# Kernel optimization log

Measured on AMD Instinct MI355X. Metric: run time of the kernel, lower is better.

Reference implementation:

```python
import jax, jax.numpy as jnp
import numpy as np

D_MODEL = 1024
N_HEADS = 16
HEAD = D_MODEL // N_HEADS  # 64


def setup_inputs() -> dict:
    key = jax.random.key(0)
    ks = jax.random.split(key, 9)
    s = 1.0 / np.sqrt(D_MODEL)
    x = jax.random.normal(ks[0], (2, 2048, D_MODEL), dtype=jnp.float32)
    Wq = jax.random.uniform(ks[1], (N_HEADS, D_MODEL, HEAD), jnp.float32, -s, s)
    bq = jax.random.uniform(ks[2], (N_HEADS, HEAD), jnp.float32, -s, s)
    Wk = jax.random.uniform(ks[3], (N_HEADS, D_MODEL, HEAD), jnp.float32, -s, s)
    bk = jax.random.uniform(ks[4], (N_HEADS, HEAD), jnp.float32, -s, s)
    Wv = jax.random.uniform(ks[5], (N_HEADS, D_MODEL, HEAD), jnp.float32, -s, s)
    bv = jax.random.uniform(ks[6], (N_HEADS, HEAD), jnp.float32, -s, s)
    Wo = jax.random.uniform(ks[7], (D_MODEL, D_MODEL), jnp.float32, -s, s)
    bo = jax.random.uniform(ks[8], (D_MODEL,), jnp.float32, -s, s)
    return {"x": x, "Wq": Wq, "bq": bq, "Wk": Wk, "bk": bk,
            "Wv": Wv, "bv": bv, "Wo": Wo, "bo": bo}


def reference(x, Wq, bq, Wk, bk, Wv, bv, Wo, bo):
    # Per-head projections, vectorized over heads: [B,S,D] x [H,D,h] -> [B,H,S,h]
    Q = jnp.einsum('bsd,hdk->bhsk', x, Wq) + bq[None, :, None, :]
    K = jnp.einsum('bsd,hdk->bhsk', x, Wk) + bk[None, :, None, :]
    V = jnp.einsum('bsd,hdk->bhsk', x, Wv) + bv[None, :, None, :]
    scores = jnp.einsum('bhqk,bhsk->bhqs', Q, K) / jnp.sqrt(jnp.float32(HEAD))
    attn = jax.nn.softmax(scores, axis=-1)  # dropout is identity in eval mode
    out = jnp.einsum('bhqs,bhsk->bhqk', attn, V)  # [B,H,S,h]
    B, H, S, h = out.shape
    out = out.transpose(0, 2, 1, 3).reshape(B, S, H * h)  # concat heads -> [B,S,D]
    return out @ Wo.T + bo if False else jnp.einsum('bsd,ed->bse', out, Wo.T.T) + bo
```

## Files before the change

kernel.cpp:

```cpp
#include <hip/hip_runtime.h>
#include <hip/hip_bf16.h>

typedef unsigned short u16;
typedef short short8 __attribute__((ext_vector_type(8)));
typedef float floatx4 __attribute__((ext_vector_type(4)));

#define MFMA16(a, b, c) __builtin_amdgcn_mfma_f32_16x16x32_bf16((a), (b), (c), 0, 0, 0)

union U128u { uint4 q; u16 s[8]; };

__device__ __forceinline__ u16 f2bf(float f) {
  union { float f; unsigned u; } v; v.f = f;
  unsigned r = v.u + 0x7fffu + ((v.u >> 16) & 1u);
  return (u16)(r >> 16);
}

__device__ __forceinline__ float bf2f(u16 s) {
  union { unsigned u; float f; } v; v.u = ((unsigned)s) << 16;
  return v.f;
}

__device__ __forceinline__ unsigned pk2(float hi, float lo) {
  union { float f; unsigned u; } a, b;
  a.f = hi; b.f = lo;
  return __builtin_amdgcn_perm(a.u + 0x8000u, b.u + 0x8000u, 0x07060302u);
}

__device__ __forceinline__ float fexp2(float x) {
#if __has_builtin(__builtin_amdgcn_exp2f)
  return __builtin_amdgcn_exp2f(x);
#else
  return exp2f(x);
#endif
}

__device__ __forceinline__ void async16(const u16* g, u16* l) {
  __builtin_amdgcn_global_load_lds(
      (const __attribute__((address_space(1))) unsigned int*)g,
      (__attribute__((address_space(3))) unsigned int*)l, 16, 0, 0);
}


__global__ __launch_bounds__(256) void prep_all(
    const float* __restrict__ x, const float* __restrict__ Wo,
    const float* __restrict__ Wq, const float* __restrict__ bq,
    const float* __restrict__ Wk, const float* __restrict__ bk,
    const float* __restrict__ Wv, const float* __restrict__ bv,
    u16* __restrict__ Xb, u16* __restrict__ Wob,
    u16* __restrict__ Wt, float* __restrict__ ball) {
  int bid = blockIdx.x;
  int tid = threadIdx.x;
  if (bid < 5120) {
    const float* src = bid < 4096 ? x : Wo;
    u16* dst = bid < 4096 ? Xb : Wob;
    int i = (bid < 4096 ? bid : bid - 4096) * 256 + tid;
    float4 v = ((const float4*)src)[i];
    union { unsigned long long ll; u16 s[4]; } o;
    o.s[0] = f2bf(v.x); o.s[1] = f2bf(v.y); o.s[2] = f2bf(v.z); o.s[3] = f2bf(v.w);
    ((unsigned long long*)dst)[i] = o.ll;
    return;
  }
  int id = (bid - 5120) * 256 + tid;
  int kk4 = id & 15;
  int d = (id >> 4) & 1023;
  int h = (id >> 14) & 15;
  int wsel = id >> 18;
  const float* W = wsel == 0 ? Wq : (wsel == 1 ? Wk : Wv);
  float4 v = *(const float4*)(W + ((size_t)(h * 1024 + d)) * 64 + kk4 * 4);
  int nb = wsel * 1024 + h * 64 + kk4 * 4;
  Wt[(size_t)(nb + 0) * 1024 + d] = f2bf(v.x);
  Wt[(size_t)(nb + 1) * 1024 + d] = f2bf(v.y);
  Wt[(size_t)(nb + 2) * 1024 + d] = f2bf(v.z);
  Wt[(size_t)(nb + 3) * 1024 + d] = f2bf(v.w);
  if (id < 3072) {
    int ws2 = id >> 10, hk = id & 1023;
    const float* bsrc = ws2 == 0 ? bq : (ws2 == 1 ? bk : bv);
    ball[id] = bsrc[hk];
  }
}


__device__ __forceinline__ void store_out(u16* p, float v) { *p = f2bf(v); }
__device__ __forceinline__ void store_out(float* p, float v) { *p = v; }

template <int BN, bool SPLITV, bool TRANS, typename OutT>
__global__ __launch_bounds__(256, 4) void gemm_bt(
    const u16* __restrict__ A, const u16* __restrict__ B,
    const float* __restrict__ bias, OutT* __restrict__ C,
    u16* __restrict__ Vtc,
    int M, int N, int K, int scaleNend, float scaleVal) {
  constexpr int TN = BN / 32;
  __shared__ __attribute__((aligned(16))) u16 As[128 * 64];
  __shared__ __attribute__((aligned(16))) u16 Bs[BN * 64];
  const int tid = threadIdx.x;
  const int w = tid >> 6, lane = tid & 63;
  const int l15 = lane & 15, l4 = lane >> 4;
  const int lin = blockIdx.x;
  const int xcd = lin & 7, sblk = lin >> 3;
  const int bm = xcd * 4 + (sblk & 3);
  const int bn = sblk >> 2;
  const int wm = (w & 1) * 64, wn = (w >> 1) * (BN / 2);

  floatx4 acc[4][TN];
#pragma unroll
  for (int i = 0; i < 4; ++i)
#pragma unroll
    for (int j = 0; j < TN; ++j) acc[i][j] = (floatx4){0.f, 0.f, 0.f, 0.f};

  for (int k0 = 0; k0 < K; k0 += 64) {
    __syncthreads();
#pragma unroll
    for (int j = 0; j < 4; ++j) {
      int i = j * 256 + tid;
      int row = i >> 3, c = (i & 7) ^ (row & 7);
      async16(A + (size_t)(bm * 128 + row) * K + k0 + c * 8, As + (j * 256 + w * 64) * 8);
    }
#pragma unroll
    for (int j = 0; j < BN / 32; ++j) {
      int i = j * 256 + tid;
      int row = i >> 3, c = (i & 7) ^ (row & 7);
      async16(B + (size_t)(bn * BN + row) * K + k0 + c * 8, Bs + (j * 256 + w * 64) * 8);
    }
    __syncthreads();
    const int sw = l15 & 7;
#pragma unroll
    for (int ks = 0; ks < 2; ++ks) {
      short8 af[4], bf[TN];
#pragma unroll
      for (int t = 0; t < 4; ++t)
        af[t] = *(const short8*)(As + (wm + t * 16 + l15) * 64 + (((ks * 4 + l4) ^ sw)) * 8);
#pragma unroll
      for (int t = 0; t < TN; ++t)
        bf[t] = *(const short8*)(Bs + (wn + t * 16 + l15) * 64 + (((ks * 4 + l4) ^ sw)) * 8);
#pragma unroll
      for (int tm = 0; tm < 4; ++tm)
#pragma unroll
        for (int tn = 0; tn < TN; ++tn)
          acc[tm][tn] = TRANS ? MFMA16(bf[tn], af[tm], acc[tm][tn])
                              : MFMA16(af[tm], bf[tn], acc[tm][tn]);
    }
  }

  if (TRANS) {
#pragma unroll
    for (int tn = 0; tn < TN; ++tn) {
      int colb = bn * BN + wn + tn * 16 + l4 * 4;
      float4 bv4 = *(const float4*)(bias + colb);
#pragma unroll
      for (int tm = 0; tm < 4; ++tm) {
        int row = bm * 128 + wm + tm * 16 + l15;
        float4 v;
        v.x = acc[tm][tn][0] + bv4.x;
        v.y = acc[tm][tn][1] + bv4.y;
        v.z = acc[tm][tn][2] + bv4.z;
        v.w = acc[tm][tn][3] + bv4.w;
        *(float4*)((float*)C + (size_t)row * N + colb) = v;
      }
    }
    return;
  }

#pragma unroll
  for (int tn = 0; tn < TN; ++tn) {
    int col = bn * BN + wn + tn * 16 + l15;
    float bv = bias[col];
    float sc = (col < scaleNend) ? scaleVal : 1.0f;
    if (!SPLITV || col < 2048) {
#pragma unroll
      for (int tm = 0; tm < 4; ++tm) {
        int row0 = bm * 128 + wm + tm * 16 + l4 * 4;
#pragma unroll
        for (int r = 0; r < 4; ++r) {
          float v = (acc[tm][tn][r] + bv) * sc;
          store_out(C + (size_t)(row0 + r) * N + col, v);
        }
      }
    } else {
      int hv = (col - 2048) >> 6, d = (col - 2048) & 63;
#pragma unroll
      for (int tm = 0; tm < 4; ++tm) {
        int row0 = bm * 128 + wm + tm * 16 + l4 * 4;
        int bb = row0 >> 11, s0 = row0 & 2047;
        union { unsigned long long ll; u16 s[4]; } o;
#pragma unroll
        for (int r = 0; r < 4; ++r) o.s[r] = f2bf(acc[tm][tn][r] + bv);
        size_t idx = ((((size_t)(bb * 16 + hv) * 128 + (s0 >> 4)) * 2 + ((s0 >> 3) & 1)) * 64 + d) * 8 +
                     (s0 & 7);
        *(unsigned long long*)(Vtc + idx) = o.ll;
      }
    }
  }
}

__global__ __launch_bounds__(256, 3) void attn_kernel(const u16* __restrict__ QKV,
                                                      const u16* __restrict__ Vtc,
                                                      u16* __restrict__ Ob) {
  __shared__ __attribute__((aligned(16))) u16 lds[4 * 5120];
  const int tid = threadIdx.x;
  const int w = tid >> 6, lane = tid & 63;
  const int l15 = lane & 15, l4 = lane >> 4;
  const int lin = blockIdx.x;
  const int xcd = lin & 7, sblk = lin >> 3;
  const int bh = xcd * 4 + (sblk & 3);
  const int q0 = (sblk >> 2) * 64;
  const int b = bh >> 4, h = bh & 15;

  u16* const Pw = lds + w * 5120;

  short8 qf[4][2];
  {
    const u16* Qb = QKV + (size_t)(b * 2048 + q0) * 3072 + h * 64;
#pragma unroll
    for (int tq = 0; tq < 4; ++tq)
#pragma unroll
      for (int s = 0; s < 2; ++s)
        qf[tq][s] = *(const short8*)(Qb + (size_t)(tq * 16 + l15) * 3072 + s * 32 + l4 * 8);
  }

  floatx4 Oacc[4][4];
#pragma unroll
  for (int i = 0; i < 4; ++i)
#pragma unroll
    for (int j = 0; j < 4; ++j) Oacc[i][j] = (floatx4){0.f, 0.f, 0.f, 0.f};
  float lpart[4] = {0.f, 0.f, 0.f, 0.f};

  const u16* const Kb = QKV + (size_t)(b * 2048) * 3072 + 1024 + h * 64;
  const u16* const Vw = Vtc + (size_t)bh * 131072 + (size_t)w * 32768;
  const int kw0 = w * 512;

  auto do_st = [&](int c, u16* pb) {
    const int key0 = kw0 + c * 32;
    short8 kf[2][2];
#pragma unroll
    for (int t = 0; t < 2; ++t)
#pragma unroll
      for (int s = 0; s < 2; ++s)
        kf[t][s] = *(const short8*)(Kb + (size_t)(key0 + t * 16 + l15) * 3072 + s * 32 + l4 * 8);
#pragma unroll
    for (int t = 0; t < 2; ++t)
#pragma unroll
      for (int tq = 0; tq < 4; ++tq) {
        floatx4 s = (floatx4){0.f, 0.f, 0.f, 0.f};
        s = MFMA16(kf[t][0], qf[tq][0], s);
        s = MFMA16(kf[t][1], qf[tq][1], s);
        float p0 = fexp2(s[0]), p1 = fexp2(s[1]), p2 = fexp2(s[2]), p3 = fexp2(s[3]);
        lpart[tq] += (p0 + p1) + (p2 + p3);
        unsigned lo = pk2(p1, p0), hi = pk2(p3, p2);
        *(unsigned long long*)(pb + (size_t)(tq * 16 + l15) * 40 + t * 16 + l4 * 4) =
            ((unsigned long long)hi << 32) | lo;
      }
  };

  auto do_pv = [&](int c, const u16* pb) {
    short8 vf[4];
#pragma unroll
    for (int td = 0; td < 4; ++td)
      vf[td] = *(const short8*)(Vw + (size_t)c * 2048 + l4 * 512 + (td * 16 + l15) * 8);
    short8 pf[4];
#pragma unroll
    for (int tq = 0; tq < 4; ++tq)
      pf[tq] = *(const short8*)(pb + (size_t)(tq * 16 + l15) * 40 + l4 * 8);
#pragma unroll
    for (int td = 0; td < 4; ++td)
#pragma unroll
      for (int tq = 0; tq < 4; ++tq) Oacc[tq][td] = MFMA16(pf[tq], vf[td], Oacc[tq][td]);
  };

  do_st(0, Pw);
#pragma unroll 1
  for (int c = 1; c < 16; ++c) {
    do_st(c, Pw + (c & 1) * 2560);
    do_pv(c - 1, Pw + ((c - 1) & 1) * 2560);
  }
  do_pv(15, Pw + 2560);

  float lr[4];
#pragma unroll
  for (int tq = 0; tq < 4; ++tq) {
    float l = lpart[tq];
    l += __shfl_xor(l, 16);
    l += __shfl_xor(l, 32);
    lr[tq] = l;
  }

#pragma unroll
  for (int tq = 0; tq < 4; ++tq)
#pragma unroll
    for (int td = 0; td < 4; ++td)
#pragma unroll
      for (int r = 0; r < 4; ++r)
        Pw[(size_t)(tq * 16 + l4 * 4 + r) * 72 + td * 16 + l15] = f2bf(Oacc[tq][td][r]);
  if (l4 == 0) {
    float* Lw = (float*)(Pw + 4608);
#pragma unroll
    for (int tq = 0; tq < 4; ++tq) Lw[tq * 16 + l15] = lr[tq];
  }
  __syncthreads();

  {
    int row = tid >> 2, c0 = (tid & 3) * 16;
    float acc[16];
#pragma unroll
    for (int j = 0; j < 16; ++j) acc[j] = 0.f;
    float lsum = 0.f;
#pragma unroll
    for (int wv = 0; wv < 4; ++wv) {
      const u16* R = lds + wv * 5120;
      lsum += ((const float*)(R + 4608))[row];
      U128u x1, x2;
      x1.q = *(const uint4*)(R + (size_t)row * 72 + c0);
      x2.q = *(const uint4*)(R + (size_t)row * 72 + c0 + 8);
#pragma unroll
      for (int j = 0; j < 8; ++j) { acc[j] += bf2f(x1.s[j]); acc[8 + j] += bf2f(x2.s[j]); }
    }
    float inv = 1.0f / lsum;
    U128u o1, o2;
#pragma unroll
    for (int j = 0; j < 8; ++j) { o1.s[j] = f2bf(acc[j] * inv); o2.s[j] = f2bf(acc[8 + j] * inv); }
    u16* Op = Ob + (size_t)(b * 2048 + q0 + row) * 1024 + h * 64 + c0;
    *(uint4*)Op = o1.q;
    *(uint4*)(Op + 8) = o2.q;
  }
}


extern "C" void kernel_launch(void* const* d_in, const int* in_sizes, int n_in,
                              void* d_out, int out_size, void* d_ws, size_t ws_size,
                              hipStream_t stream) {
  const float* x  = (const float*)d_in[0];
  const float* Wq = (const float*)d_in[1];
  const float* bq = (const float*)d_in[2];
  const float* Wk = (const float*)d_in[3];
  const float* bk = (const float*)d_in[4];
  const float* Wv = (const float*)d_in[5];
  const float* bv = (const float*)d_in[6];
  const float* Wo = (const float*)d_in[7];
  const float* bo = (const float*)d_in[8];

  char* p = (char*)d_ws;
  u16* Xb   = (u16*)p; p += (size_t)4096 * 1024 * 2;
  u16* Wt   = (u16*)p; p += (size_t)3072 * 1024 * 2;
  u16* QKV  = (u16*)p; p += (size_t)4096 * 3072 * 2;
  u16* Vtc  = (u16*)p; p += (size_t)32 * 128 * 2 * 64 * 8 * 2;
  u16* Ob   = (u16*)p; p += (size_t)4096 * 1024 * 2;
  u16* Wob  = (u16*)p; p += (size_t)1024 * 1024 * 2;
  float* ball = (float*)p; p += 3072 * sizeof(float);

  const float qscale = 0.125f * 1.4426950408889634f;

  prep_all<<<8192, 256, 0, stream>>>(x, Wo, Wq, bq, Wk, bk, Wv, bv, Xb, Wob, Wt, ball);
  gemm_bt<96, true, false, u16><<<1024, 256, 0, stream>>>(Xb, Wt, ball, QKV, Vtc,
                                                          4096, 3072, 1024, 1024, qscale);
  attn_kernel<<<1024, 256, 0, stream>>>(QKV, Vtc, Ob);
  gemm_bt<64, false, true, float><<<512, 256, 0, stream>>>(Ob, Wob, bo, (float*)d_out, nullptr,
                                                           4096, 1024, 1024, 0, 1.0f);
}
```

Before: 200.3 us.

## Prefetch K fragments one chunk ahead in attention; add dedicated 64x64 output GEMM

The attention loop now loads the next chunk's K fragments into registers before computing the current scores, so global load latency overlaps with MFMA and exp work. The output projection moves from the generic gemm_bt template (512 blocks) to a new 64x64-tile kernel with swizzled LDS, async loads and 1024 blocks, aimed at better occupancy and wave count. The prefetch raises register pressure, and the new GEMM loop is single-buffered with two barriers per k-step.

Result: faster. 192.2 us (-4.0%).

```diff
diff --git a/kernel.cpp b/kernel.cpp
--- a/kernel.cpp
+++ b/kernel.cpp
@@ -192,6 +192,76 @@
   }
 }
 
+__global__ __launch_bounds__(256, 4) void gemm_out64(
+    const u16* __restrict__ A, const u16* __restrict__ B,
+    const float* __restrict__ bias, float* __restrict__ C) {
+  __shared__ __attribute__((aligned(16))) u16 As[64 * 64];
+  __shared__ __attribute__((aligned(16))) u16 Bs[64 * 64];
+  const int tid = threadIdx.x;
+  const int w = tid >> 6, lane = tid & 63;
+  const int l15 = lane & 15, l4 = lane >> 4;
+  const int lin = blockIdx.x;
+  const int xcd = lin & 7, sblk = lin >> 3;
+  const int bm = xcd * 8 + (sblk & 7);
+  const int bn = sblk >> 3;
+  const int wm = (w & 1) * 32, wn = (w >> 1) * 32;
+
+  floatx4 acc[2][2];
+#pragma unroll
+  for (int i = 0; i < 2; ++i)
+#pragma unroll
+    for (int j = 0; j < 2; ++j) acc[i][j] = (floatx4){0.f, 0.f, 0.f, 0.f};
+
+  for (int k0 = 0; k0 < 1024; k0 += 64) {
+    __syncthreads();
+#pragma unroll
+    for (int j = 0; j < 2; ++j) {
+      int i = j * 256 + tid;
+      int row = i >> 3, c = (i & 7) ^ (row & 7);
+      async16(A + (size_t)(bm * 64 + row) * 1024 + k0 + c * 8, As + (j * 256 + w * 64) * 8);
+    }
+#pragma unroll
+    for (int j = 0; j < 2; ++j) {
+      int i = j * 256 + tid;
+      int row = i >> 3, c = (i & 7) ^ (row & 7);
+      async16(B + (size_t)(bn * 64 + row) * 1024 + k0 + c * 8, Bs + (j * 256 + w * 64) * 8);
+    }
+    __syncthreads();
+    const int sw = l15 & 7;
+#pragma unroll
+    for (int ks = 0; ks < 2; ++ks) {
+      short8 af[2], bf[2];
+#pragma unroll
+      for (int t = 0; t < 2; ++t)
+        af[t] = *(const short8*)(As + (wm + t * 16 + l15) * 64 + (((ks * 4 + l4) ^ sw)) * 8);
+#pragma unroll
+      for (int t = 0; t < 2; ++t)
+        bf[t] = *(const short8*)(Bs + (wn + t * 16 + l15) * 64 + (((ks * 4 + l4) ^ sw)) * 8);
+#pragma unroll
+      for (int tm = 0; tm < 2; ++tm)
+#pragma unroll
+        for (int tn = 0; tn < 2; ++tn)
+          acc[tm][tn] = MFMA16(bf[tn], af[tm], acc[tm][tn]);
+    }
+  }
+
+#pragma unroll
+  for (int tn = 0; tn < 2; ++tn) {
+    int colb = bn * 64 + wn + tn * 16 + l4 * 4;
+    float4 bv4 = *(const float4*)(bias + colb);
+#pragma unroll
+    for (int tm = 0; tm < 2; ++tm) {
+      int row = bm * 64 + wm + tm * 16 + l15;
+      float4 v;
+      v.x = acc[tm][tn][0] + bv4.x;
+      v.y = acc[tm][tn][1] + bv4.y;
+      v.z = acc[tm][tn][2] + bv4.z;
+      v.w = acc[tm][tn][3] + bv4.w;
+      *(float4*)(C + (size_t)row * 1024 + colb) = v;
+    }
+  }
+}
+
 __global__ __launch_bounds__(256, 3) void attn_kernel(const u16* __restrict__ QKV,
                                                       const u16* __restrict__ Vtc,
                                                       u16* __restrict__ Ob) {
@@ -228,14 +298,16 @@
   const u16* const Vw = Vtc + (size_t)bh * 131072 + (size_t)w * 32768;
   const int kw0 = w * 512;
 
-  auto do_st = [&](int c, u16* pb) {
+  auto load_kf = [&](int c, short8 kf[2][2]) {
     const int key0 = kw0 + c * 32;
-    short8 kf[2][2];
 #pragma unroll
     for (int t = 0; t < 2; ++t)
 #pragma unroll
       for (int s = 0; s < 2; ++s)
         kf[t][s] = *(const short8*)(Kb + (size_t)(key0 + t * 16 + l15) * 3072 + s * 32 + l4 * 8);
+  };
+
+  auto do_st = [&](const short8 kf[2][2], u16* pb) {
 #pragma unroll
     for (int t = 0; t < 2; ++t)
 #pragma unroll
@@ -266,12 +338,30 @@
       for (int tq = 0; tq < 4; ++tq) Oacc[tq][td] = MFMA16(pf[tq], vf[td], Oacc[tq][td]);
   };
 
-  do_st(0, Pw);
+  short8 kfc[2][2];
+  load_kf(0, kfc);
+  {
+    short8 kfn[2][2];
+    load_kf(1, kfn);
+    do_st(kfc, Pw);
+#pragma unroll
+    for (int t = 0; t < 2; ++t)
+#pragma unroll
+      for (int s = 0; s < 2; ++s) kfc[t][s] = kfn[t][s];
+  }
 #pragma unroll 1
-  for (int c = 1; c < 16; ++c) {
-    do_st(c, Pw + (c & 1) * 2560);
+  for (int c = 1; c < 15; ++c) {
+    short8 kfn[2][2];
+    load_kf(c + 1, kfn);
+    do_st(kfc, Pw + (c & 1) * 2560);
     do_pv(c - 1, Pw + ((c - 1) & 1) * 2560);
-  }
+#pragma unroll
+    for (int t = 0; t < 2; ++t)
+#pragma unroll
+      for (int s = 0; s < 2; ++s) kfc[t][s] = kfn[t][s];
+  }
+  do_st(kfc, Pw + 2560);
+  do_pv(14, Pw);
   do_pv(15, Pw + 2560);
 
   float lr[4];
@@ -352,6 +442,5 @@
   gemm_bt<96, true, false, u16><<<1024, 256, 0, stream>>>(Xb, Wt, ball, QKV, Vtc,
                                                           4096, 3072, 1024, 1024, qscale);
   attn_kernel<<<1024, 256, 0, stream>>>(QKV, Vtc, Ob);
-  gemm_bt<64, false, true, float><<<512, 256, 0, stream>>>(Ob, Wob, bo, (float*)d_out, nullptr,
-                                                           4096, 1024, 1024, 0, 1.0f);
-}
+  gemm_out64<<<1024, 256, 0, stream>>>(Ob, Wob, bo, (float*)d_out);
+}
```
